# Kernel tuning notes

Hardware: AMD Instinct MI355X
Metric: run time of the kernel (lower is better)

The kernel has to match this reference:

```python
import jax, jax.numpy as jnp
import numpy as np

SMOOTHING = 0.1
PAD_IDX = 0

def setup_inputs() -> dict:
    key = jax.random.key(0)
    k1, k2 = jax.random.split(key)
    B, S, V = 2, 2048, 32000
    pred = jax.random.normal(k1, (B, S, V), dtype=jnp.float32)
    target = jax.random.randint(k2, (B, S), 0, V, dtype=jnp.int64)
    return {"pred": pred, "target": target}

def reference(pred, target):
    B, S, V = pred.shape
    # smoothed target distribution: onehot*(1-s) + s/V
    onehot = jax.nn.one_hot(target, V, dtype=pred.dtype)
    t_smooth = onehot * (1.0 - SMOOTHING) + SMOOTHING / V
    logp = jax.nn.log_softmax(pred, axis=-1)
    # KLDivLoss(reduction='none'): target * (log(target) - input)
    kld = t_smooth * (jnp.log(t_smooth) - logp)  # [B, S, V]
    mask = (target != PAD_IDX).astype(pred.dtype)[..., None]  # [B, S, 1]
    kld = kld * mask
    # 'mean' reduction in the module: sum over everything / number of non-pad tokens
    return jnp.sum(kld) / jnp.sum(mask)
```

## Files before the change

### kernel.cpp

```cpp
#include <hip/hip_runtime.h>
#include <math.h>

#define SMOOTH 0.1f
#define PAD_IDX 0

__global__ void __launch_bounds__(256)
row_kernel(const float* __restrict__ pred,
           const int* __restrict__ target,
           float* __restrict__ ws, int V) {
    const int row = blockIdx.x;
    const int tid = threadIdx.x;
    const float* __restrict__ p = pred + (long long)row * V;
    const int tgt = target[row];

    const float L2E   = 1.4426950408889634f;
    const float BIAS  = 4.0f;
    const float BIAS2 = BIAS * L2E;

#define EXP4(v) ( __builtin_amdgcn_exp2f(fmaf((v).x, L2E, -BIAS2)) \
                + __builtin_amdgcn_exp2f(fmaf((v).y, L2E, -BIAS2)) \
                + __builtin_amdgcn_exp2f(fmaf((v).z, L2E, -BIAS2)) \
                + __builtin_amdgcn_exp2f(fmaf((v).w, L2E, -BIAS2)) )
#define SUM4(v) (((v).x + (v).y) + ((v).z + (v).w))

    float s0 = 0.0f, s1 = 0.0f, s2 = 0.0f, s3 = 0.0f;
    float x0 = 0.0f, x1 = 0.0f, x2 = 0.0f, x3 = 0.0f;

    const int V4 = V >> 2;
    const float4* __restrict__ p4 = (const float4*)p;

    int i = tid;
    for (; i + 768 < V4; i += 1024) {
        float4 a = p4[i];
        float4 b = p4[i + 256];
        float4 c = p4[i + 512];
        float4 d = p4[i + 768];
        x0 += SUM4(a);
        x1 += SUM4(b);
        x2 += SUM4(c);
        x3 += SUM4(d);
        s0 += EXP4(a);
        s1 += EXP4(b);
        s2 += EXP4(c);
        s3 += EXP4(d);
    }
    for (; i < V4; i += 256) {
        float4 a = p4[i];
        x0 += SUM4(a);
        s0 += EXP4(a);
    }
    for (int j = (V4 << 2) + tid; j < V; j += 256) {
        float x = p[j];
        x0 += x;
        s0 += __builtin_amdgcn_exp2f(fmaf(x, L2E, -BIAS2));
    }

    float s  = (s0 + s1) + (s2 + s3);
    float sx = (x0 + x1) + (x2 + x3);

    for (int off = 32; off > 0; off >>= 1) {
        s  += __shfl_down(s, off, 64);
        sx += __shfl_down(sx, off, 64);
    }

    __shared__ float ss[4], sxs[4];
    const int wid = tid >> 6, lane = tid & 63;
    if (lane == 0) { ss[wid] = s; sxs[wid] = sx; }
    __syncthreads();

    if (tid == 0) {
        for (int w = 1; w < 4; ++w) { s += ss[w]; sx += sxs[w]; }
        const float LN2 = 0.6931471805599453f;
        float lse = BIAS + LN2 * __builtin_amdgcn_logf(s);
        float pt = p[tgt];

        double lo = (double)SMOOTH / (double)V;
        double hi = 1.0 - (double)SMOOTH + lo;
        float C = (float)((double)(V - 1) * lo * log(lo) + hi * log(hi));

        float sum_logp = sx - (float)V * lse;
        float kld = C - (SMOOTH / (float)V) * sum_logp
                      - (1.0f - SMOOTH) * (pt - lse);
        float mask = (tgt != PAD_IDX) ? 1.0f : 0.0f;
        float2 o; o.x = kld * mask; o.y = mask;
        ((float2*)ws)[row] = o;
    }
#undef EXP4
#undef SUM4
}

__global__ void __launch_bounds__(256)
reduce_kernel(const float* __restrict__ ws, float* __restrict__ out, int rows) {
    const int tid = threadIdx.x;
    const float2* __restrict__ w2 = (const float2*)ws;
    float sk = 0.0f, sm = 0.0f;
    for (int i = tid; i < rows; i += 256) {
        float2 v = w2[i];
        sk += v.x;
        sm += v.y;
    }
    for (int off = 32; off > 0; off >>= 1) {
        sk += __shfl_down(sk, off, 64);
        sm += __shfl_down(sm, off, 64);
    }
    __shared__ float a[4], b[4];
    const int wid = tid >> 6, lane = tid & 63;
    if (lane == 0) { a[wid] = sk; b[wid] = sm; }
    __syncthreads();
    if (tid == 0) {
        for (int w = 1; w < 4; ++w) { sk += a[w]; sm += b[w]; }
        out[0] = sk / sm;
    }
}

extern "C" void kernel_launch(void* const* d_in, const int* in_sizes, int n_in,
                              void* d_out, int out_size, void* d_ws, size_t ws_size,
                              hipStream_t stream) {
    const float* pred  = (const float*)d_in[0];
    const int*  target = (const int*)d_in[1];
    const int rows = in_sizes[1];
    const int V    = in_sizes[0] / rows;
    float* ws  = (float*)d_ws;
    float* out = (float*)d_out;

    hipLaunchKernelGGL(row_kernel, dim3(rows), dim3(256), 0, stream,
                       pred, target, ws, V);
    hipLaunchKernelGGL(reduce_kernel, dim3(1), dim3(256), 0, stream,
                       ws, out, rows);
}
```

Measured before the change: 664.6 us.

## Split each row across two blocks and finalize per-row loss in reduce kernel

Each row is now processed by two blocks, each covering half the vocabulary. Each block writes its partial exp-sum, value sum, target logit and mask to the workspace, and the reduce kernel merges the halves and computes the per-row KL term. The loads also become nontemporal. The aim is more blocks in flight and more memory parallelism on a bandwidth-bound pass, at the cost of twice the workspace writes and a heavier single-block final reduction.

```diff
diff --git a/kernel.cpp b/kernel.cpp
--- a/kernel.cpp
+++ b/kernel.cpp
@@ -4,18 +4,32 @@
 #define SMOOTH 0.1f
 #define PAD_IDX 0
 
+
+typedef float f32x4 __attribute__((ext_vector_type(4)));
+
 __global__ void __launch_bounds__(256)
 row_kernel(const float* __restrict__ pred,
            const int* __restrict__ target,
            float* __restrict__ ws, int V) {
-    const int row = blockIdx.x;
-    const int tid = threadIdx.x;
+    const int row   = blockIdx.x >> 1;
+    const int chunk = blockIdx.x & 1;
+    const int tid   = threadIdx.x;
     const float* __restrict__ p = pred + (long long)row * V;
     const int tgt = target[row];
 
     const float L2E   = 1.4426950408889634f;
     const float BIAS  = 4.0f;
     const float BIAS2 = BIAS * L2E;
+
+    const int V4   = V >> 2;
+    const int C4   = V4 >> 1;
+    const int base = chunk * C4;
+    const int n    = chunk ? (V4 - C4) : C4;
+    const f32x4* __restrict__ p4 = ((const f32x4*)p) + base;
+
+    float ptv = 0.0f;
+    const bool owner = chunk ? (tgt >= 4 * C4) : (tgt < 4 * C4);
+    if (owner && tid == 0) ptv = p[tgt];
 
 #define EXP4(v) ( __builtin_amdgcn_exp2f(fmaf((v).x, L2E, -BIAS2)) \
                 + __builtin_amdgcn_exp2f(fmaf((v).y, L2E, -BIAS2)) \
@@ -26,15 +40,12 @@
     float s0 = 0.0f, s1 = 0.0f, s2 = 0.0f, s3 = 0.0f;
     float x0 = 0.0f, x1 = 0.0f, x2 = 0.0f, x3 = 0.0f;
 
-    const int V4 = V >> 2;
-    const float4* __restrict__ p4 = (const float4*)p;
-
-    int i = tid;
-    for (; i + 768 < V4; i += 1024) {
-        float4 a = p4[i];
-        float4 b = p4[i + 256];
-        float4 c = p4[i + 512];
-        float4 d = p4[i + 768];
+    int k = tid;
+    for (; k + 768 < n; k += 1024) {
+        f32x4 a = __builtin_nontemporal_load(p4 + k);
+        f32x4 b = __builtin_nontemporal_load(p4 + k + 256);
+        f32x4 c = __builtin_nontemporal_load(p4 + k + 512);
+        f32x4 d = __builtin_nontemporal_load(p4 + k + 768);
         x0 += SUM4(a);
         x1 += SUM4(b);
         x2 += SUM4(c);
@@ -44,15 +55,18 @@
         s2 += EXP4(c);
         s3 += EXP4(d);
     }
-    for (; i < V4; i += 256) {
-        float4 a = p4[i];
+#pragma unroll 4
+    for (; k < n; k += 256) {
+        f32x4 a = __builtin_nontemporal_load(p4 + k);
         x0 += SUM4(a);
         s0 += EXP4(a);
     }
-    for (int j = (V4 << 2) + tid; j < V; j += 256) {
-        float x = p[j];
-        x0 += x;
-        s0 += __builtin_amdgcn_exp2f(fmaf(x, L2E, -BIAS2));
+    if (chunk) {
+        for (int j = (V4 << 2) + tid; j < V; j += 256) {
+            float x = p[j];
+            x0 += x;
+            s0 += __builtin_amdgcn_exp2f(fmaf(x, L2E, -BIAS2));
+        }
     }
 
     float s  = (s0 + s1) + (s2 + s3);
@@ -70,45 +84,51 @@
 
     if (tid == 0) {
         for (int w = 1; w < 4; ++w) { s += ss[w]; sx += sxs[w]; }
-        const float LN2 = 0.6931471805599453f;
-        float lse = BIAS + LN2 * __builtin_amdgcn_logf(s);
-        float pt = p[tgt];
-
-        double lo = (double)SMOOTH / (double)V;
-        double hi = 1.0 - (double)SMOOTH + lo;
-        float C = (float)((double)(V - 1) * lo * log(lo) + hi * log(hi));
-
-        float sum_logp = sx - (float)V * lse;
-        float kld = C - (SMOOTH / (float)V) * sum_logp
-                      - (1.0f - SMOOTH) * (pt - lse);
         float mask = (tgt != PAD_IDX) ? 1.0f : 0.0f;
-        float2 o; o.x = kld * mask; o.y = mask;
-        ((float2*)ws)[row] = o;
+        f32x4 o; o.x = s; o.y = sx; o.z = ptv; o.w = mask;
+        ((f32x4*)ws)[blockIdx.x] = o;
     }
 #undef EXP4
 #undef SUM4
 }
 
-__global__ void __launch_bounds__(256)
-reduce_kernel(const float* __restrict__ ws, float* __restrict__ out, int rows) {
+__global__ void __launch_bounds__(1024)
+reduce_kernel(const float* __restrict__ ws, float* __restrict__ out,
+              int rows, int V) {
     const int tid = threadIdx.x;
-    const float2* __restrict__ w2 = (const float2*)ws;
+    const f32x4* __restrict__ w4 = (const f32x4*)ws;
+
+    const float BIAS = 4.0f;
+    const float LN2  = 0.6931471805599453f;
+    double lo = (double)SMOOTH / (double)V;
+    double hi = 1.0 - (double)SMOOTH + lo;
+    const float C = (float)((double)(V - 1) * lo * log(lo) + hi * log(hi));
+
     float sk = 0.0f, sm = 0.0f;
-    for (int i = tid; i < rows; i += 256) {
-        float2 v = w2[i];
-        sk += v.x;
-        sm += v.y;
+    for (int r = tid; r < rows; r += 1024) {
+        f32x4 a = w4[2 * r];
+        f32x4 b = w4[2 * r + 1];
+        float s    = a.x + b.x;
+        float sx   = a.y + b.y;
+        float pt   = a.z + b.z;
+        float mask = a.w;
+        float lse = BIAS + LN2 * __builtin_amdgcn_logf(s);
+        float sum_logp = sx - (float)V * lse;
+        float kld = C - (SMOOTH / (float)V) * sum_logp
+                      - (1.0f - SMOOTH) * (pt - lse);
+        sk += kld * mask;
+        sm += mask;
     }
     for (int off = 32; off > 0; off >>= 1) {
         sk += __shfl_down(sk, off, 64);
         sm += __shfl_down(sm, off, 64);
     }
-    __shared__ float a[4], b[4];
+    __shared__ float a16[16], b16[16];
     const int wid = tid >> 6, lane = tid & 63;
-    if (lane == 0) { a[wid] = sk; b[wid] = sm; }
+    if (lane == 0) { a16[wid] = sk; b16[wid] = sm; }
     __syncthreads();
     if (tid == 0) {
-        for (int w = 1; w < 4; ++w) { sk += a[w]; sm += b[w]; }
+        for (int w = 1; w < 16; ++w) { sk += a16[w]; sm += b16[w]; }
         out[0] = sk / sm;
     }
 }
@@ -123,8 +143,8 @@
     float* ws  = (float*)d_ws;
     float* out = (float*)d_out;
 
-    hipLaunchKernelGGL(row_kernel, dim3(rows), dim3(256), 0, stream,
+    hipLaunchKernelGGL(row_kernel, dim3(rows * 2), dim3(256), 0, stream,
                        pred, target, ws, V);
-    hipLaunchKernelGGL(reduce_kernel, dim3(1), dim3(256), 0, stream,
-                       ws, out, rows);
+    hipLaunchKernelGGL(reduce_kernel, dim3(1), dim3(1024), 0, stream,
+                       ws, out, rows, V);
 }
```

New measurement: 630.0 us. 1.05x faster.
